# Kernel tuning notes

Hardware: AMD Instinct MI355X
Metric: run time of the kernel (lower is better)

The kernel has to match this reference:

```python
import jax, jax.numpy as jnp
import numpy as np

N_ROWS = 16384
INP_UNITS = 8192
OUT_UNITS = 128
NNZ = 1_048_576


def setup_inputs() -> dict:
    key = jax.random.key(0)
    k1, k2, k3, k4 = jax.random.split(key, 4)
    values = jax.random.normal(k1, (NNZ,), dtype=jnp.float32)
    w = jax.random.normal(k2, (INP_UNITS, OUT_UNITS), dtype=jnp.float32)
    # COO indices, rows sorted as in a canonical tf.SparseTensor
    rows = jnp.sort(jax.random.randint(k3, (NNZ,), 0, N_ROWS, dtype=jnp.int32)).astype(jnp.int64)
    cols = jax.random.randint(k4, (NNZ,), 0, INP_UNITS, dtype=jnp.int32).astype(jnp.int64)
    return {"values": values, "w": w, "rows": rows, "cols": cols, "n_rows": N_ROWS}


def reference(values, w, rows, cols, n_rows):
    # sparse (COO) x dense matmul: out[r, :] = sum_{k: rows[k]==r} values[k] * w[cols[k], :]
    contrib = values[:, None] * w[cols]  # [nnz, out_units]
    return jax.ops.segment_sum(contrib, rows, num_segments=n_rows)
```

## Files before the change

### kernel.cpp

```cpp
#include <hip/hip_runtime.h>
#include <hip/hip_fp16.h>

#define OUT_UNITS 128

__global__ void convert_w(const float4* __restrict__ w4,
                          uint2* __restrict__ wh, int n4) {
    int i = blockIdx.x * blockDim.x + threadIdx.x;
    if (i >= n4) return;
    float4 f = w4[i];
    __half2 h01 = __floats2half2_rn(f.x, f.y);
    __half2 h23 = __floats2half2_rn(f.z, f.w);
    wh[i] = make_uint2(*(unsigned*)&h01, *(unsigned*)&h23);
}

__global__ void build_row_starts(const int* __restrict__ rows,
                                 int* __restrict__ row_start,
                                 int nnz, int n_rows) {
    int k = blockIdx.x * blockDim.x + threadIdx.x;
    if (k >= nnz) return;
    int cur = rows[k];
    if (k == 0) {
        for (int r = 0; r <= cur; ++r) row_start[r] = 0;
    } else {
        int prev = rows[k - 1];
        for (int r = prev + 1; r <= cur; ++r) row_start[r] = k;
    }
    if (k == nnz - 1) {
        for (int r = cur + 1; r <= n_rows; ++r) row_start[r] = nnz;
    }
}

__global__ __launch_bounds__(256, 4)
void spmm_row_wave(const float* __restrict__ vals,
                   const __half* __restrict__ wh,
                   const int* __restrict__ cols,
                   const int* __restrict__ row_start,
                   float* __restrict__ out,
                   int n_rows) {
    __shared__ int2 cvbuf[4][64];

    const int wave = __builtin_amdgcn_readfirstlane((int)(threadIdx.x >> 6));
    const int lane = threadIdx.x & 63;
    const int r    = blockIdx.x * 4 + wave;
    if (r >= n_rows) return;

    const int start   = row_start[r];
    const int end     = row_start[r + 1];
    const int quarter = lane >> 4;
    const int sub     = lane & 15;
    const char* __restrict__ whb = (const char*)wh;
    const int loff = sub << 4;
    int2* cv = cvbuf[wave];

    float4 accA = make_float4(0.f, 0.f, 0.f, 0.f);
    float4 accB = make_float4(0.f, 0.f, 0.f, 0.f);

    for (int base = start; base < end; base += 64) {
        const int navail = min(64, end - base);
        const int idx = base + min(lane, navail - 1);
        int   c_l = cols[idx];
        float v_l = (lane < navail) ? vals[idx] : 0.f;
        cv[lane] = make_int2(c_l, __float_as_int(v_l));

        const int nquad  = (navail + 3) >> 2;
        const int nquad4 = (nquad + 3) & ~3;

        for (int t = 0; t < nquad4; t += 4) {
            int2 p0 = cv[4 * (t + 0) + quarter];
            int2 p1 = cv[4 * (t + 1) + quarter];
            int2 p2 = cv[4 * (t + 2) + quarter];
            int2 p3 = cv[4 * (t + 3) + quarter];
            uint4 q0 = *(const uint4*)(whb + (((size_t)(unsigned)p0.x) << 8) + loff);
            uint4 q1 = *(const uint4*)(whb + (((size_t)(unsigned)p1.x) << 8) + loff);
            uint4 q2 = *(const uint4*)(whb + (((size_t)(unsigned)p2.x) << 8) + loff);
            uint4 q3 = *(const uint4*)(whb + (((size_t)(unsigned)p3.x) << 8) + loff);
#pragma unroll
            for (int j = 0; j < 4; ++j) {
                uint4 q = (j == 0) ? q0 : (j == 1) ? q1 : (j == 2) ? q2 : q3;
                float v = __int_as_float(((j == 0) ? p0 : (j == 1) ? p1
                                        : (j == 2) ? p2 : p3).y);
                const __half2* h = (const __half2*)&q;
                float2 f0 = __half22float2(h[0]);
                float2 f1 = __half22float2(h[1]);
                float2 f2 = __half22float2(h[2]);
                float2 f3 = __half22float2(h[3]);
                accA.x = fmaf(v, f0.x, accA.x); accA.y = fmaf(v, f0.y, accA.y);
                accA.z = fmaf(v, f1.x, accA.z); accA.w = fmaf(v, f1.y, accA.w);
                accB.x = fmaf(v, f2.x, accB.x); accB.y = fmaf(v, f2.y, accB.y);
                accB.z = fmaf(v, f3.x, accB.z); accB.w = fmaf(v, f3.y, accB.w);
            }
        }
    }

#pragma unroll
    for (int d = 16; d <= 32; d <<= 1) {
        accA.x += __shfl_xor(accA.x, d); accA.y += __shfl_xor(accA.y, d);
        accA.z += __shfl_xor(accA.z, d); accA.w += __shfl_xor(accA.w, d);
        accB.x += __shfl_xor(accB.x, d); accB.y += __shfl_xor(accB.y, d);
        accB.z += __shfl_xor(accB.z, d); accB.w += __shfl_xor(accB.w, d);
    }

    if (quarter == 0) {
        float4* o = (float4*)(out + (size_t)r * OUT_UNITS + sub * 8);
        o[0] = accA;
        o[1] = accB;
    }
}

extern "C" void kernel_launch(void* const* d_in, const int* in_sizes, int n_in,
                              void* d_out, int out_size, void* d_ws, size_t ws_size,
                              hipStream_t stream) {
    const float* vals = (const float*)d_in[0];
    const float* w    = (const float*)d_in[1];
    const int*   rows = (const int*)d_in[2];
    const int*   cols = (const int*)d_in[3];
    float* out = (float*)d_out;

    const int nnz    = in_sizes[0];
    const int n_rows = out_size / OUT_UNITS;
    const int w_n    = in_sizes[1];

    int*    row_start = (int*)d_ws;
    __half* wh        = (__half*)((char*)d_ws + (128 << 10));

    convert_w<<<(w_n / 4 + 255) / 256, 256, 0, stream>>>(
        (const float4*)w, (uint2*)wh, w_n / 4);
    build_row_starts<<<(nnz + 255) / 256, 256, 0, stream>>>(rows, row_start, nnz, n_rows);
    spmm_row_wave<<<(n_rows + 3) / 4, 256, 0, stream>>>(vals, wh, cols, row_start, out, n_rows);
}
```

Measured before the change: 89.69 us.

## Fuse prep kernels and software-pipeline W gathers in SpMM inner loop

```diff
diff --git a/kernel.cpp b/kernel.cpp
--- a/kernel.cpp
+++ b/kernel.cpp
@@ -3,30 +3,27 @@
 
 #define OUT_UNITS 128
 
-__global__ void convert_w(const float4* __restrict__ w4,
-                          uint2* __restrict__ wh, int n4) {
+__global__ void prep(const float4* __restrict__ w4, uint2* __restrict__ wh, int n4,
+                     const int* __restrict__ rows, int* __restrict__ row_start,
+                     int nnz, int n_rows) {
     int i = blockIdx.x * blockDim.x + threadIdx.x;
-    if (i >= n4) return;
-    float4 f = w4[i];
-    __half2 h01 = __floats2half2_rn(f.x, f.y);
-    __half2 h23 = __floats2half2_rn(f.z, f.w);
-    wh[i] = make_uint2(*(unsigned*)&h01, *(unsigned*)&h23);
-}
-
-__global__ void build_row_starts(const int* __restrict__ rows,
-                                 int* __restrict__ row_start,
-                                 int nnz, int n_rows) {
-    int k = blockIdx.x * blockDim.x + threadIdx.x;
-    if (k >= nnz) return;
-    int cur = rows[k];
-    if (k == 0) {
-        for (int r = 0; r <= cur; ++r) row_start[r] = 0;
-    } else {
-        int prev = rows[k - 1];
-        for (int r = prev + 1; r <= cur; ++r) row_start[r] = k;
+    if (i < n4) {
+        float4 f = w4[i];
+        __half2 h01 = __floats2half2_rn(f.x, f.y);
+        __half2 h23 = __floats2half2_rn(f.z, f.w);
+        wh[i] = make_uint2(*(unsigned*)&h01, *(unsigned*)&h23);
     }
-    if (k == nnz - 1) {
-        for (int r = cur + 1; r <= n_rows; ++r) row_start[r] = nnz;
+    if (i < nnz) {
+        int cur = rows[i];
+        if (i == 0) {
+            for (int r = 0; r <= cur; ++r) row_start[r] = 0;
+        } else {
+            int prev = rows[i - 1];
+            for (int r = prev + 1; r <= cur; ++r) row_start[r] = i;
+        }
+        if (i == nnz - 1) {
+            for (int r = cur + 1; r <= n_rows; ++r) row_start[r] = nnz;
+        }
     }
 }
 
@@ -65,21 +62,26 @@
         const int nquad  = (navail + 3) >> 2;
         const int nquad4 = (nquad + 3) & ~3;
 
-        for (int t = 0; t < nquad4; t += 4) {
-            int2 p0 = cv[4 * (t + 0) + quarter];
-            int2 p1 = cv[4 * (t + 1) + quarter];
-            int2 p2 = cv[4 * (t + 2) + quarter];
-            int2 p3 = cv[4 * (t + 3) + quarter];
-            uint4 q0 = *(const uint4*)(whb + (((size_t)(unsigned)p0.x) << 8) + loff);
-            uint4 q1 = *(const uint4*)(whb + (((size_t)(unsigned)p1.x) << 8) + loff);
-            uint4 q2 = *(const uint4*)(whb + (((size_t)(unsigned)p2.x) << 8) + loff);
-            uint4 q3 = *(const uint4*)(whb + (((size_t)(unsigned)p3.x) << 8) + loff);
+        int2  pA[4];
+        uint4 qA[4];
+#pragma unroll
+        for (int j = 0; j < 4; ++j) pA[j] = cv[4 * j + quarter];
+#pragma unroll
+        for (int j = 0; j < 4; ++j)
+            qA[j] = *(const uint4*)(whb + (((size_t)(unsigned)pA[j].x) << 8) + loff);
+
+        for (int t = 4; t < nquad4; t += 4) {
+            int2  pB[4];
+            uint4 qB[4];
+#pragma unroll
+            for (int j = 0; j < 4; ++j) pB[j] = cv[4 * (t + j) + quarter];
+#pragma unroll
+            for (int j = 0; j < 4; ++j)
+                qB[j] = *(const uint4*)(whb + (((size_t)(unsigned)pB[j].x) << 8) + loff);
 #pragma unroll
             for (int j = 0; j < 4; ++j) {
-                uint4 q = (j == 0) ? q0 : (j == 1) ? q1 : (j == 2) ? q2 : q3;
-                float v = __int_as_float(((j == 0) ? p0 : (j == 1) ? p1
-                                        : (j == 2) ? p2 : p3).y);
-                const __half2* h = (const __half2*)&q;
+                float v = __int_as_float(pA[j].y);
+                const __half2* h = (const __half2*)&qA[j];
                 float2 f0 = __half22float2(h[0]);
                 float2 f1 = __half22float2(h[1]);
                 float2 f2 = __half22float2(h[2]);
@@ -89,6 +91,22 @@
                 accB.x = fmaf(v, f2.x, accB.x); accB.y = fmaf(v, f2.y, accB.y);
                 accB.z = fmaf(v, f3.x, accB.z); accB.w = fmaf(v, f3.y, accB.w);
             }
+#pragma unroll
+            for (int j = 0; j < 4; ++j) { pA[j] = pB[j]; qA[j] = qB[j]; }
+        }
+
+#pragma unroll
+        for (int j = 0; j < 4; ++j) {
+            float v = __int_as_float(pA[j].y);
+            const __half2* h = (const __half2*)&qA[j];
+            float2 f0 = __half22float2(h[0]);
+            float2 f1 = __half22float2(h[1]);
+            float2 f2 = __half22float2(h[2]);
+            float2 f3 = __half22float2(h[3]);
+            accA.x = fmaf(v, f0.x, accA.x); accA.y = fmaf(v, f0.y, accA.y);
+            accA.z = fmaf(v, f1.x, accA.z); accA.w = fmaf(v, f1.y, accA.w);
+            accB.x = fmaf(v, f2.x, accB.x); accB.y = fmaf(v, f2.y, accB.y);
+            accB.z = fmaf(v, f3.x, accB.z); accB.w = fmaf(v, f3.y, accB.w);
         }
     }
 
@@ -119,12 +137,13 @@
     const int nnz    = in_sizes[0];
     const int n_rows = out_size / OUT_UNITS;
     const int w_n    = in_sizes[1];
+    const int n4     = w_n / 4;
 
     int*    row_start = (int*)d_ws;
     __half* wh        = (__half*)((char*)d_ws + (128 << 10));
 
-    convert_w<<<(w_n / 4 + 255) / 256, 256, 0, stream>>>(
-        (const float4*)w, (uint2*)wh, w_n / 4);
-    build_row_starts<<<(nnz + 255) / 256, 256, 0, stream>>>(rows, row_start, nnz, n_rows);
+    const int prep_threads = (nnz > n4) ? nnz : n4;
+    prep<<<(prep_threads + 255) / 256, 256, 0, stream>>>(
+        (const float4*)w, (uint2*)wh, n4, rows, row_start, nnz, n_rows);
     spmm_row_wave<<<(n_rows + 3) / 4, 256, 0, stream>>>(vals, wh, cols, row_start, out, n_rows);
 }
```

Measured after the change: 87.86 us. 2.0% less time.
